# Performance work log

Measured on AMD Instinct MI355X. Metric: run time of the kernel, lower is better.

The kernel has to match this reference:

```python
import jax, jax.numpy as jnp
import numpy as np

N = 4096
IN_F = 256
OUT_F = 32
H = 8
NEG_SLOPE = 0.2
EDGE_P = 0.004  # avg degree ~16


def setup_inputs() -> dict:
    key = jax.random.key(0)
    k1, k2, k3, k4, k5 = jax.random.split(key, 5)
    x = jax.random.normal(k1, (N, IN_F), dtype=jnp.float32)
    adj = jax.random.bernoulli(k2, EDGE_P, (N, N))  # bool sparse-ish adjacency
    # xavier-uniform-ish scales
    w_scale = np.sqrt(6.0 / (IN_F + OUT_F))
    a_scale = np.sqrt(6.0 / (OUT_F + 1))
    W = jax.random.uniform(k3, (H, IN_F, OUT_F), jnp.float32, -w_scale, w_scale)
    a_src = jax.random.uniform(k4, (H, OUT_F), jnp.float32, -a_scale, a_scale)
    a_dst = jax.random.uniform(k5, (H, OUT_F), jnp.float32, -a_scale, a_scale)
    bias = jnp.zeros((H * OUT_F,), dtype=jnp.float32)
    return {"x": x, "adj": adj, "W": W, "a_src": a_src, "a_dst": a_dst, "bias": bias}


def reference(x, adj, W, a_src, a_dst, bias):
    n = x.shape[0]
    # adjacency mask with self-loops, (N, N)
    mask = adj | jnp.eye(n, dtype=bool)
    # Wh: (H, N, OUT_F)
    Wh = jnp.einsum('hif,ni->hnf', W, x)
    # per-node attention logits, (H, N)
    e_src = jnp.einsum('hnf,hf->hn', Wh, a_src)
    e_dst = jnp.einsum('hnf,hf->hn', Wh, a_dst)
    # additive scores, (H, N, N): row i attends over columns j
    e = e_src[:, :, None] + e_dst[:, None, :]
    e = jnp.where(e >= 0, e, NEG_SLOPE * e)  # LeakyReLU
    e = jnp.where(mask[None], e, -jnp.inf)
    alpha = jax.nn.softmax(e, axis=-1)
    # dropout p=0.6 is a no-op in eval mode
    out = jnp.einsum('hnm,hmf->hnf', alpha, Wh)
    # concat heads: (N, H*OUT_F)
    out = jnp.transpose(out, (1, 0, 2)).reshape(n, -1)
    return out + bias
```

## Files before the change

### kernel.cpp

```cpp
#include <hip/hip_runtime.h>
#include <hip/hip_bf16.h>
#include <stdint.h>

#define N_NODES 4096
#define IN_F 256
#define OUT_F 32
#define H 8
#define HF 256
#define NPB 8
#define XPAD 14
#define MAXK 64
#define NWH 512
#define NBUILD 1024

typedef __hip_bfloat16 bf16;
__device__ __forceinline__ float b2f(bf16 v) { return __bfloat162float(v); }

__device__ __forceinline__ int detect_f32m(const void* xv, int t) {
    uint16_t u = ((const uint16_t*)xv)[t & 63];
    bf16 v = *(bf16*)&u;
    float f = b2f(v);
    int wild = !(fabsf(f) < 100.0f);
    return __popcll(__ballot(wild)) > 4;
}

union SmemU {
    float xl[IN_F][XPAD];
    struct {
        int nbr[4][MAXK];
        int s[3];
    } b;
};

__global__ __launch_bounds__(256) void fused_kernel(
    const void* __restrict__ xv, const void* __restrict__ Wv,
    const void* __restrict__ asv, const void* __restrict__ adv,
    const uint32_t* __restrict__ adj,
    float* __restrict__ Wh, float* __restrict__ esrc, float* __restrict__ edst,
    int* __restrict__ nbrs, int* __restrict__ cnts)
{
    __shared__ SmemU sm;
    const int t = threadIdx.x;

    if (blockIdx.x >= NWH) {
        const int w = t >> 6, lane = t & 63;
        const int i = (blockIdx.x - NWH) * 4 + w;
        if (t < 3) sm.b.s[t] = 0;
        __syncthreads();
        int E = 0, F = 0, G = 0;
        #pragma unroll
        for (int i2 = 0; i2 < 16; ++i2) {
            uint32_t wd = adj[t + i2 * 256];
            if (wd >> 8) E++;
            uint32_t lo = wd & 0xFFFFu, hi = wd >> 16;
            if (lo == 0x3F80u || hi == 0x3F80u) F++;
            if (lo) G++;
        }
        if (E) atomicAdd(&sm.b.s[0], E);
        if (F) atomicAdd(&sm.b.s[1], F);
        if (G) atomicAdd(&sm.b.s[2], G);
        __syncthreads();
        int amode;
        {
            int Eb = sm.b.s[0], Fb = sm.b.s[1], Gb = sm.b.s[2];
            if (Eb == 0)                amode = 0;
            else if (Fb > 0 && Gb == 0) amode = 0;
            else if (Fb > 0)            amode = 1;
            else                        amode = 2;
        }
        int cnt = 0;
        int* mynbr = sm.b.nbr[w];
        const unsigned long long lmask_lt = (lane == 63) ? ~0ull >> 1
                                          : (1ull << lane) - 1;
        auto wpush = [&](bool pred, int col) {
            pred = pred && (col != i);
            unsigned long long mask = __ballot(pred);
            if (mask) {
                if (pred) {
                    int p = cnt + __popcll(mask & ((1ull << lane) - 1));
                    if (p < MAXK) mynbr[p] = col;
                }
                cnt += __popcll(mask);
            }
        };

        if (amode == 0) {
            const int4* row = (const int4*)(adj + (size_t)i * N_NODES);
            #pragma unroll
            for (int rr = 0; rr < 4; ++rr) {
                int4 v[4];
                #pragma unroll
                for (int q = 0; q < 4; ++q) v[q] = row[lane + (rr * 4 + q) * 64];
                #pragma unroll
                for (int q = 0; q < 4; ++q) {
                    int j0 = (lane + (rr * 4 + q) * 64) * 4;
                    wpush(v[q].x != 0, j0);
                    wpush(v[q].y != 0, j0 + 1);
                    wpush(v[q].z != 0, j0 + 2);
                    wpush(v[q].w != 0, j0 + 3);
                }
            }
        } else if (amode == 1) {
            const int4* row = (const int4*)((const uint16_t*)adj + (size_t)i * N_NODES);
            #pragma unroll
            for (int rr = 0; rr < 2; ++rr) {
                int4 v[4];
                #pragma unroll
                for (int q = 0; q < 4; ++q) v[q] = row[lane + (rr * 4 + q) * 64];
                #pragma unroll
                for (int q = 0; q < 4; ++q) {
                    int j0 = (lane + (rr * 4 + q) * 64) * 8;
                    uint32_t u0 = (uint32_t)v[q].x, u1 = (uint32_t)v[q].y;
                    uint32_t u2 = (uint32_t)v[q].z, u3 = (uint32_t)v[q].w;
                    wpush((u0 & 0xFFFFu) != 0, j0);     wpush((u0 >> 16) != 0, j0 + 1);
                    wpush((u1 & 0xFFFFu) != 0, j0 + 2); wpush((u1 >> 16) != 0, j0 + 3);
                    wpush((u2 & 0xFFFFu) != 0, j0 + 4); wpush((u2 >> 16) != 0, j0 + 5);
                    wpush((u3 & 0xFFFFu) != 0, j0 + 6); wpush((u3 >> 16) != 0, j0 + 7);
                }
            }
        } else {
            const int4* row = (const int4*)((const uint8_t*)adj + (size_t)i * N_NODES);
            int4 v[4];
            #pragma unroll
            for (int q = 0; q < 4; ++q) v[q] = row[lane + q * 64];
            #pragma unroll
            for (int q = 0; q < 4; ++q) {
                int j0 = (lane + q * 64) * 16;
                uint32_t u[4] = {(uint32_t)v[q].x, (uint32_t)v[q].y,
                                 (uint32_t)v[q].z, (uint32_t)v[q].w};
                #pragma unroll
                for (int b = 0; b < 4; ++b) {
                    uint32_t uu = u[b]; int c0 = j0 + 4 * b;
                    wpush((uu & 0x000000FFu) != 0, c0);
                    wpush((uu & 0x0000FF00u) != 0, c0 + 1);
                    wpush((uu & 0x00FF0000u) != 0, c0 + 2);
                    wpush((uu & 0xFF000000u) != 0, c0 + 3);
                }
            }
        }
        if (lane == 0 && cnt < MAXK) mynbr[cnt] = i;
        cnt += 1;
        const int K = cnt < MAXK ? cnt : MAXK;
        __builtin_amdgcn_wave_barrier();
        if (lane < K) nbrs[(size_t)i * MAXK + lane] = mynbr[lane];
        if (lane == 0) cnts[i] = K;
        return;
    }

    const int f32m = detect_f32m(xv, t);
    const int n0 = blockIdx.x * NPB;

    if (f32m) {
        const float* x = (const float*)xv + (size_t)n0 * IN_F;
        #pragma unroll
        for (int r = 0; r < NPB; ++r) sm.xl[t][r] = x[(size_t)r * IN_F + t];
    } else {
        const bf16* x = (const bf16*)xv + (size_t)n0 * IN_F;
        #pragma unroll
        for (int r = 0; r < NPB; ++r) sm.xl[t][r] = b2f(x[(size_t)r * IN_F + t]);
    }
    __syncthreads();

    const int rg = t >> 6;
    const int cg = t & 63;
    const int h  = cg >> 3;
    const int f0 = (cg & 7) * 4;

    float acc[2][4];
    #pragma unroll
    for (int r = 0; r < 2; ++r)
        #pragma unroll
        for (int j = 0; j < 4; ++j) acc[r][j] = 0.f;

    if (f32m) {
        const float* Wp = (const float*)Wv + (size_t)h * IN_F * OUT_F + f0;
        #pragma unroll 8
        for (int i = 0; i < IN_F; ++i) {
            const float4 w4 = *(const float4*)&Wp[(size_t)i * OUT_F];
            const float x0 = sm.xl[i][rg * 2];
            const float x1 = sm.xl[i][rg * 2 + 1];
            acc[0][0] += x0 * w4.x; acc[0][1] += x0 * w4.y;
            acc[0][2] += x0 * w4.z; acc[0][3] += x0 * w4.w;
            acc[1][0] += x1 * w4.x; acc[1][1] += x1 * w4.y;
            acc[1][2] += x1 * w4.z; acc[1][3] += x1 * w4.w;
        }
    } else {
        const bf16* Wp = (const bf16*)Wv + (size_t)h * IN_F * OUT_F + f0;
        #pragma unroll 8
        for (int i = 0; i < IN_F; ++i) {
            const ushort4 wu = *(const ushort4*)&Wp[(size_t)i * OUT_F];
            float w0 = b2f(*(bf16*)&wu.x), w1 = b2f(*(bf16*)&wu.y);
            float w2 = b2f(*(bf16*)&wu.z), w3 = b2f(*(bf16*)&wu.w);
            const float x0 = sm.xl[i][rg * 2];
            const float x1 = sm.xl[i][rg * 2 + 1];
            acc[0][0] += x0 * w0; acc[0][1] += x0 * w1;
            acc[0][2] += x0 * w2; acc[0][3] += x0 * w3;
            acc[1][0] += x1 * w0; acc[1][1] += x1 * w1;
            acc[1][2] += x1 * w2; acc[1][3] += x1 * w3;
        }
    }

    float as0, as1, as2, as3, ad0, ad1, ad2, ad3;
    if (f32m) {
        const float4 a4 = *(const float4*)&((const float*)asv)[h * OUT_F + f0];
        const float4 b4 = *(const float4*)&((const float*)adv)[h * OUT_F + f0];
        as0 = a4.x; as1 = a4.y; as2 = a4.z; as3 = a4.w;
        ad0 = b4.x; ad1 = b4.y; ad2 = b4.z; ad3 = b4.w;
    } else {
        const ushort4 a4 = *(const ushort4*)&((const bf16*)asv)[h * OUT_F + f0];
        const ushort4 b4 = *(const ushort4*)&((const bf16*)adv)[h * OUT_F + f0];
        as0 = b2f(*(bf16*)&a4.x); as1 = b2f(*(bf16*)&a4.y);
        as2 = b2f(*(bf16*)&a4.z); as3 = b2f(*(bf16*)&a4.w);
        ad0 = b2f(*(bf16*)&b4.x); ad1 = b2f(*(bf16*)&b4.y);
        ad2 = b2f(*(bf16*)&b4.z); ad3 = b2f(*(bf16*)&b4.w);
    }

    #pragma unroll
    for (int r = 0; r < 2; ++r) {
        const int n = n0 + rg * 2 + r;
        *(float4*)&Wh[(size_t)n * HF + cg * 4] =
            make_float4(acc[r][0], acc[r][1], acc[r][2], acc[r][3]);
        float vs = acc[r][0] * as0 + acc[r][1] * as1 + acc[r][2] * as2 + acc[r][3] * as3;
        float vd = acc[r][0] * ad0 + acc[r][1] * ad1 + acc[r][2] * ad2 + acc[r][3] * ad3;
        vs += __shfl_down(vs, 4, 8); vs += __shfl_down(vs, 2, 8); vs += __shfl_down(vs, 1, 8);
        vd += __shfl_down(vd, 4, 8); vd += __shfl_down(vd, 2, 8); vd += __shfl_down(vd, 1, 8);
        if ((cg & 7) == 0) {
            esrc[(size_t)n * H + h] = vs;
            edst[(size_t)n * H + h] = vd;
        }
    }
}

__global__ __launch_bounds__(256) void gat2_kernel(
    const float* __restrict__ Wh, const float* __restrict__ esrc,
    const float* __restrict__ edst, const int* __restrict__ nbrs,
    const int* __restrict__ cnts, const void* __restrict__ xv,
    const void* __restrict__ biasv, void* __restrict__ outv)
{
    __shared__ float sc[4][MAXK * H];
    __shared__ int   nbw[4][MAXK];

    const int t = threadIdx.x;
    const int w = t >> 6, lane = t & 63;
    const int i = blockIdx.x * 4 + w;
    const int f32m = detect_f32m(xv, t);
    const int K = min(cnts[i], MAXK);

    if (lane < K) {
        int j = nbrs[(size_t)i * MAXK + lane];
        nbw[w][lane] = j;
        const float4* e4 = (const float4*)edst;
        const float4* s4 = (const float4*)esrc;
        float4 ej0 = e4[j * 2], ej1 = e4[j * 2 + 1];
        float4 si0 = s4[i * 2], si1 = s4[i * 2 + 1];
        float lg[8] = {si0.x + ej0.x, si0.y + ej0.y, si0.z + ej0.z, si0.w + ej0.w,
                       si1.x + ej1.x, si1.y + ej1.y, si1.z + ej1.z, si1.w + ej1.w};
        #pragma unroll
        for (int h = 0; h < 8; ++h) {
            float s = lg[h];
            sc[w][lane * 8 + h] = s >= 0.f ? s : 0.2f * s;
        }
    }
    __syncthreads();

    float m = -1e30f, inv = 0.f;
    if (lane < 8) {
        for (int k = 0; k < K; ++k) m = fmaxf(m, sc[w][k * 8 + lane]);
        float sum = 0.f;
        for (int k = 0; k < K; ++k) sum += __expf(sc[w][k * 8 + lane] - m);
        inv = 1.f / sum;
    }
    const int h = lane >> 3, f0c = lane * 4;
    const float mh  = __shfl(m, h, 64);
    const float ivh = __shfl(inv, h, 64);

    float a0 = 0.f, a1 = 0.f, a2 = 0.f, a3 = 0.f;
    #pragma unroll 4
    for (int k = 0; k < K; ++k) {
        float e = __expf(sc[w][k * 8 + h] - mh);
        const float4 v = *(const float4*)&Wh[(size_t)nbw[w][k] * HF + f0c];
        a0 += e * v.x; a1 += e * v.y; a2 += e * v.z; a3 += e * v.w;
    }

    float b0, b1, b2, b3;
    if (f32m) {
        const float4 b4 = ((const float4*)biasv)[lane];
        b0 = b4.x; b1 = b4.y; b2 = b4.z; b3 = b4.w;
    } else {
        const ushort4 b4 = ((const ushort4*)biasv)[lane];
        b0 = b2f(*(bf16*)&b4.x); b1 = b2f(*(bf16*)&b4.y);
        b2 = b2f(*(bf16*)&b4.z); b3 = b2f(*(bf16*)&b4.w);
    }
    a0 = a0 * ivh + b0; a1 = a1 * ivh + b1;
    a2 = a2 * ivh + b2; a3 = a3 * ivh + b3;

    if (f32m) {
        ((float4*)outv)[(size_t)i * 64 + lane] = make_float4(a0, a1, a2, a3);
    } else {
        bf16 h0 = __float2bfloat16(a0), h1 = __float2bfloat16(a1);
        bf16 h2 = __float2bfloat16(a2), h3 = __float2bfloat16(a3);
        ushort4 o;
        o.x = *(uint16_t*)&h0; o.y = *(uint16_t*)&h1;
        o.z = *(uint16_t*)&h2; o.w = *(uint16_t*)&h3;
        ((ushort4*)outv)[(size_t)i * 64 + lane] = o;
    }
}

extern "C" void kernel_launch(void* const* d_in, const int* in_sizes, int n_in,
                              void* d_out, int out_size, void* d_ws, size_t ws_size,
                              hipStream_t stream) {
    const void* x     = d_in[0];
    const void* adj   = d_in[1];
    const void* W     = d_in[2];
    const void* a_src = d_in[3];
    const void* a_dst = d_in[4];
    const void* bias  = d_in[5];

    float* Wh   = (float*)((char*)d_ws + 256);
    float* esrc = Wh + (size_t)N_NODES * HF;
    float* edst = esrc + (size_t)N_NODES * H;
    int*   cnts = (int*)(edst + (size_t)N_NODES * H);
    int*   nbrs = cnts + N_NODES;

    fused_kernel<<<NWH + NBUILD, 256, 0, stream>>>(
        x, W, a_src, a_dst, (const uint32_t*)adj, Wh, esrc, edst, nbrs, cnts);
    gat2_kernel<<<N_NODES / 4, 256, 0, stream>>>(
        Wh, esrc, edst, nbrs, cnts, x, bias, d_out);
}
```

Baseline: 127.5 us.

## Move neighbor-list construction from first kernel into attention kernel

The adjacency scan that builds per-row neighbor lists moves out of the first kernel and into the aggregation kernel, so each wave scans its own row and uses the list straight from shared memory. The first kernel keeps only the Wh projection and one extra block that detects the adjacency dtype and writes a mode flag to workspace. This drops the global round-trip of neighbor indices and counts and the 1024 builder blocks. In exchange, the adjacency scan now runs after the Wh kernel instead of alongside it, and the loads switch from int4 vectors to scalar words.

```diff
diff --git a/kernel.cpp b/kernel.cpp
--- a/kernel.cpp
+++ b/kernel.cpp
@@ -11,7 +11,6 @@
 #define XPAD 14
 #define MAXK 64
 #define NWH 512
-#define NBUILD 1024
 
 typedef __hip_bfloat16 bf16;
 __device__ __forceinline__ float b2f(bf16 v) { return __bfloat162float(v); }
@@ -24,28 +23,18 @@
     return __popcll(__ballot(wild)) > 4;
 }
 
-union SmemU {
-    float xl[IN_F][XPAD];
-    struct {
-        int nbr[4][MAXK];
-        int s[3];
-    } b;
-};
-
-__global__ __launch_bounds__(256) void fused_kernel(
+__global__ __launch_bounds__(256) void wh_kernel(
     const void* __restrict__ xv, const void* __restrict__ Wv,
     const void* __restrict__ asv, const void* __restrict__ adv,
-    const uint32_t* __restrict__ adj,
-    float* __restrict__ Wh, float* __restrict__ esrc, float* __restrict__ edst,
-    int* __restrict__ nbrs, int* __restrict__ cnts)
+    const uint32_t* __restrict__ adj, int* __restrict__ modes,
+    float* __restrict__ Wh, float* __restrict__ esrc, float* __restrict__ edst)
 {
-    __shared__ SmemU sm;
     const int t = threadIdx.x;
-
-    if (blockIdx.x >= NWH) {
-        const int w = t >> 6, lane = t & 63;
-        const int i = (blockIdx.x - NWH) * 4 + w;
-        if (t < 3) sm.b.s[t] = 0;
+    const int w = t >> 6, lane = t & 63;
+
+    if (blockIdx.x == NWH) {
+        __shared__ int s[3];
+        if (t < 3) s[t] = 0;
         __syncthreads();
         int E = 0, F = 0, G = 0;
         #pragma unroll
@@ -56,113 +45,38 @@
             if (lo == 0x3F80u || hi == 0x3F80u) F++;
             if (lo) G++;
         }
-        if (E) atomicAdd(&sm.b.s[0], E);
-        if (F) atomicAdd(&sm.b.s[1], F);
-        if (G) atomicAdd(&sm.b.s[2], G);
+        if (E) atomicAdd(&s[0], E);
+        if (F) atomicAdd(&s[1], F);
+        if (G) atomicAdd(&s[2], G);
         __syncthreads();
-        int amode;
-        {
-            int Eb = sm.b.s[0], Fb = sm.b.s[1], Gb = sm.b.s[2];
-            if (Eb == 0)                amode = 0;
-            else if (Fb > 0 && Gb == 0) amode = 0;
-            else if (Fb > 0)            amode = 1;
-            else                        amode = 2;
-        }
-        int cnt = 0;
-        int* mynbr = sm.b.nbr[w];
-        const unsigned long long lmask_lt = (lane == 63) ? ~0ull >> 1
-                                          : (1ull << lane) - 1;
-        auto wpush = [&](bool pred, int col) {
-            pred = pred && (col != i);
-            unsigned long long mask = __ballot(pred);
-            if (mask) {
-                if (pred) {
-                    int p = cnt + __popcll(mask & ((1ull << lane) - 1));
-                    if (p < MAXK) mynbr[p] = col;
-                }
-                cnt += __popcll(mask);
-            }
-        };
-
-        if (amode == 0) {
-            const int4* row = (const int4*)(adj + (size_t)i * N_NODES);
-            #pragma unroll
-            for (int rr = 0; rr < 4; ++rr) {
-                int4 v[4];
-                #pragma unroll
-                for (int q = 0; q < 4; ++q) v[q] = row[lane + (rr * 4 + q) * 64];
-                #pragma unroll
-                for (int q = 0; q < 4; ++q) {
-                    int j0 = (lane + (rr * 4 + q) * 64) * 4;
-                    wpush(v[q].x != 0, j0);
-                    wpush(v[q].y != 0, j0 + 1);
-                    wpush(v[q].z != 0, j0 + 2);
-                    wpush(v[q].w != 0, j0 + 3);
-                }
-            }
-        } else if (amode == 1) {
-            const int4* row = (const int4*)((const uint16_t*)adj + (size_t)i * N_NODES);
-            #pragma unroll
-            for (int rr = 0; rr < 2; ++rr) {
-                int4 v[4];
-                #pragma unroll
-                for (int q = 0; q < 4; ++q) v[q] = row[lane + (rr * 4 + q) * 64];
-                #pragma unroll
-                for (int q = 0; q < 4; ++q) {
-                    int j0 = (lane + (rr * 4 + q) * 64) * 8;
-                    uint32_t u0 = (uint32_t)v[q].x, u1 = (uint32_t)v[q].y;
-                    uint32_t u2 = (uint32_t)v[q].z, u3 = (uint32_t)v[q].w;
-                    wpush((u0 & 0xFFFFu) != 0, j0);     wpush((u0 >> 16) != 0, j0 + 1);
-                    wpush((u1 & 0xFFFFu) != 0, j0 + 2); wpush((u1 >> 16) != 0, j0 + 3);
-                    wpush((u2 & 0xFFFFu) != 0, j0 + 4); wpush((u2 >> 16) != 0, j0 + 5);
-                    wpush((u3 & 0xFFFFu) != 0, j0 + 6); wpush((u3 >> 16) != 0, j0 + 7);
-                }
-            }
-        } else {
-            const int4* row = (const int4*)((const uint8_t*)adj + (size_t)i * N_NODES);
-            int4 v[4];
-            #pragma unroll
-            for (int q = 0; q < 4; ++q) v[q] = row[lane + q * 64];
-            #pragma unroll
-            for (int q = 0; q < 4; ++q) {
-                int j0 = (lane + q * 64) * 16;
-                uint32_t u[4] = {(uint32_t)v[q].x, (uint32_t)v[q].y,
-                                 (uint32_t)v[q].z, (uint32_t)v[q].w};
-                #pragma unroll
-                for (int b = 0; b < 4; ++b) {
-                    uint32_t uu = u[b]; int c0 = j0 + 4 * b;
-                    wpush((uu & 0x000000FFu) != 0, c0);
-                    wpush((uu & 0x0000FF00u) != 0, c0 + 1);
-                    wpush((uu & 0x00FF0000u) != 0, c0 + 2);
-                    wpush((uu & 0xFF000000u) != 0, c0 + 3);
-                }
-            }
-        }
-        if (lane == 0 && cnt < MAXK) mynbr[cnt] = i;
-        cnt += 1;
-        const int K = cnt < MAXK ? cnt : MAXK;
-        __builtin_amdgcn_wave_barrier();
-        if (lane < K) nbrs[(size_t)i * MAXK + lane] = mynbr[lane];
-        if (lane == 0) cnts[i] = K;
+        if (t == 0) {
+            int amode;
+            if (s[0] == 0)               amode = 0;
+            else if (s[1] > 0 && !s[2])  amode = 0;
+            else if (s[1] > 0)           amode = 1;
+            else                         amode = 2;
+            modes[0] = amode;
+        }
         return;
     }
 
+    __shared__ float xl[IN_F][XPAD];
     const int f32m = detect_f32m(xv, t);
     const int n0 = blockIdx.x * NPB;
 
     if (f32m) {
         const float* x = (const float*)xv + (size_t)n0 * IN_F;
         #pragma unroll
-        for (int r = 0; r < NPB; ++r) sm.xl[t][r] = x[(size_t)r * IN_F + t];
+        for (int r = 0; r < NPB; ++r) xl[t][r] = x[(size_t)r * IN_F + t];
     } else {
         const bf16* x = (const bf16*)xv + (size_t)n0 * IN_F;
         #pragma unroll
-        for (int r = 0; r < NPB; ++r) sm.xl[t][r] = b2f(x[(size_t)r * IN_F + t]);
+        for (int r = 0; r < NPB; ++r) xl[t][r] = b2f(x[(size_t)r * IN_F + t]);
     }
     __syncthreads();
 
-    const int rg = t >> 6;
-    const int cg = t & 63;
+    const int rg = w;
+    const int cg = lane;
     const int h  = cg >> 3;
     const int f0 = (cg & 7) * 4;
 
@@ -177,8 +91,8 @@
         #pragma unroll 8
         for (int i = 0; i < IN_F; ++i) {
             const float4 w4 = *(const float4*)&Wp[(size_t)i * OUT_F];
-            const float x0 = sm.xl[i][rg * 2];
-            const float x1 = sm.xl[i][rg * 2 + 1];
+            const float x0 = xl[i][rg * 2];
+            const float x1 = xl[i][rg * 2 + 1];
             acc[0][0] += x0 * w4.x; acc[0][1] += x0 * w4.y;
             acc[0][2] += x0 * w4.z; acc[0][3] += x0 * w4.w;
             acc[1][0] += x1 * w4.x; acc[1][1] += x1 * w4.y;
@@ -191,8 +105,8 @@
             const ushort4 wu = *(const ushort4*)&Wp[(size_t)i * OUT_F];
             float w0 = b2f(*(bf16*)&wu.x), w1 = b2f(*(bf16*)&wu.y);
             float w2 = b2f(*(bf16*)&wu.z), w3 = b2f(*(bf16*)&wu.w);
-            const float x0 = sm.xl[i][rg * 2];
-            const float x1 = sm.xl[i][rg * 2 + 1];
+            const float x0 = xl[i][rg * 2];
+            const float x1 = xl[i][rg * 2 + 1];
             acc[0][0] += x0 * w0; acc[0][1] += x0 * w1;
             acc[0][2] += x0 * w2; acc[0][3] += x0 * w3;
             acc[1][0] += x1 * w0; acc[1][1] += x1 * w1;
@@ -231,10 +145,10 @@
     }
 }
 
-__global__ __launch_bounds__(256) void gat2_kernel(
-    const float* __restrict__ Wh, const float* __restrict__ esrc,
-    const float* __restrict__ edst, const int* __restrict__ nbrs,
-    const int* __restrict__ cnts, const void* __restrict__ xv,
+__global__ __launch_bounds__(256) void gat3_kernel(
+    const uint32_t* __restrict__ adj, const float* __restrict__ Wh,
+    const float* __restrict__ esrc, const float* __restrict__ edst,
+    const int* __restrict__ modes, const void* __restrict__ xv,
     const void* __restrict__ biasv, void* __restrict__ outv)
 {
     __shared__ float sc[4][MAXK * H];
@@ -244,11 +158,81 @@
     const int w = t >> 6, lane = t & 63;
     const int i = blockIdx.x * 4 + w;
     const int f32m = detect_f32m(xv, t);
-    const int K = min(cnts[i], MAXK);
+    const int amode = modes[0];
+
+    int cnt = 0;
+    int* mynbr = nbw[w];
+    const unsigned long long ltmask = (1ull << lane) - 1;
+
+    if (amode == 0) {
+        const uint32_t* row = adj + (size_t)i * N_NODES;
+        #pragma unroll 8
+        for (int g = 0; g < 64; ++g) {
+            int col = g * 64 + lane;
+            uint32_t wd = row[col];
+            bool pred = (wd != 0) & (col != i);
+            unsigned long long mask = __ballot(pred);
+            if (mask) {
+                if (pred) {
+                    int p = cnt + __popcll(mask & ltmask);
+                    if (p < MAXK) mynbr[p] = col;
+                }
+                cnt += __popcll(mask);
+            }
+        }
+    } else if (amode == 1) {
+        const uint32_t* row = (const uint32_t*)((const uint16_t*)adj + (size_t)i * N_NODES);
+        #pragma unroll 8
+        for (int g = 0; g < 32; ++g) {
+            int wi = g * 64 + lane;
+            uint32_t wd = row[wi];
+            int c0 = wi * 2;
+            bool p0 = ((wd & 0xFFFFu) != 0) & (c0 != i);
+            bool p1 = ((wd >> 16)     != 0) & (c0 + 1 != i);
+            unsigned long long m0 = __ballot(p0);
+            if (m0) {
+                if (p0) {
+                    int p = cnt + __popcll(m0 & ltmask);
+                    if (p < MAXK) mynbr[p] = c0;
+                }
+                cnt += __popcll(m0);
+            }
+            unsigned long long m1 = __ballot(p1);
+            if (m1) {
+                if (p1) {
+                    int p = cnt + __popcll(m1 & ltmask);
+                    if (p < MAXK) mynbr[p] = c0 + 1;
+                }
+                cnt += __popcll(m1);
+            }
+        }
+    } else {
+        const uint32_t* row = (const uint32_t*)((const uint8_t*)adj + (size_t)i * N_NODES);
+        #pragma unroll 4
+        for (int g = 0; g < 16; ++g) {
+            int wi = g * 64 + lane;
+            uint32_t wd = row[wi];
+            int c0 = wi * 4;
+            #pragma unroll
+            for (int b = 0; b < 4; ++b) {
+                bool p = (((wd >> (8 * b)) & 0xFFu) != 0) & (c0 + b != i);
+                unsigned long long m = __ballot(p);
+                if (m) {
+                    if (p) {
+                        int q = cnt + __popcll(m & ltmask);
+                        if (q < MAXK) mynbr[q] = c0 + b;
+                    }
+                    cnt += __popcll(m);
+                }
+            }
+        }
+    }
+    if (lane == 0 && cnt < MAXK) mynbr[cnt] = i;
+    cnt += 1;
+    const int K = cnt < MAXK ? cnt : MAXK;
 
     if (lane < K) {
-        int j = nbrs[(size_t)i * MAXK + lane];
-        nbw[w][lane] = j;
+        int j = mynbr[lane];
         const float4* e4 = (const float4*)edst;
         const float4* s4 = (const float4*)esrc;
         float4 ej0 = e4[j * 2], ej1 = e4[j * 2 + 1];
@@ -261,7 +245,6 @@
             sc[w][lane * 8 + h] = s >= 0.f ? s : 0.2f * s;
         }
     }
-    __syncthreads();
 
     float m = -1e30f, inv = 0.f;
     if (lane < 8) {
@@ -278,7 +261,7 @@
     #pragma unroll 4
     for (int k = 0; k < K; ++k) {
         float e = __expf(sc[w][k * 8 + h] - mh);
-        const float4 v = *(const float4*)&Wh[(size_t)nbw[w][k] * HF + f0c];
+        const float4 v = *(const float4*)&Wh[(size_t)mynbr[k] * HF + f0c];
         a0 += e * v.x; a1 += e * v.y; a2 += e * v.z; a3 += e * v.w;
     }
 
@@ -316,14 +299,13 @@
     const void* a_dst = d_in[4];
     const void* bias  = d_in[5];
 
-    float* Wh   = (float*)((char*)d_ws + 256);
-    float* esrc = Wh + (size_t)N_NODES * HF;
-    float* edst = esrc + (size_t)N_NODES * H;
-    int*   cnts = (int*)(edst + (size_t)N_NODES * H);
-    int*   nbrs = cnts + N_NODES;
-
-    fused_kernel<<<NWH + NBUILD, 256, 0, stream>>>(
-        x, W, a_src, a_dst, (const uint32_t*)adj, Wh, esrc, edst, nbrs, cnts);
-    gat2_kernel<<<N_NODES / 4, 256, 0, stream>>>(
-        Wh, esrc, edst, nbrs, cnts, x, bias, d_out);
+    int*   modes = (int*)d_ws;
+    float* Wh    = (float*)((char*)d_ws + 256);
+    float* esrc  = Wh + (size_t)N_NODES * HF;
+    float* edst  = esrc + (size_t)N_NODES * H;
+
+    wh_kernel<<<NWH + 1, 256, 0, stream>>>(
+        x, W, a_src, a_dst, (const uint32_t*)adj, modes, Wh, esrc, edst);
+    gat3_kernel<<<N_NODES / 4, 256, 0, stream>>>(
+        (const uint32_t*)adj, Wh, esrc, edst, modes, x, bias, d_out);
 }
```

New measurement: 152.7 us. 19.8% more time.
